# Performance work log

Hardware: AMD Instinct MI355X
Metric: run time of the kernel (lower is better)

The kernel has to match this reference:

```python
import jax, jax.numpy as jnp
import numpy as np

C = 256; G = 16; GC = C // G; K = 3; P = K * K
N = 4; H = 64; W = 64
PAD = 1; OFFSET_SCALE = 1.0; LN_EPS = 1e-5


def setup_inputs() -> dict:
    key = jax.random.key(0)
    ks = jax.random.split(key, 8)
    s = 0.02
    return {
        "x": jax.random.normal(ks[0], (N, C, H, W), jnp.float32),
        "dw_w": jax.random.normal(ks[1], (C, 1, K, K), jnp.float32) * s,
        "dw_b": jnp.zeros((C,), jnp.float32),
        "ln_g": jnp.ones((C,), jnp.float32),
        "ln_b": jnp.zeros((C,), jnp.float32),
        "off_w": jax.random.normal(ks[2], (C, G * P * 2), jnp.float32) * s,
        "off_b": jnp.zeros((G * P * 2,), jnp.float32),
        "mask_w": jax.random.normal(ks[3], (C, G * P), jnp.float32) * s,
        "mask_b": jnp.zeros((G * P,), jnp.float32),
        "inp_w": jax.random.normal(ks[4], (C, C), jnp.float32) * s,
        "inp_b": jnp.zeros((C,), jnp.float32),
        "out_w": jax.random.normal(ks[5], (C, C), jnp.float32) * s,
        "out_b": jnp.zeros((C,), jnp.float32),
    }


def _dcnv3_nchw(x, dw_w, dw_b, ln_g, ln_b, off_w, off_b, mask_w, mask_b,
                inp_w, inp_b, out_w, out_b):
    # NCHW -> NHWC (wrapper permute)
    xn = jnp.transpose(x, (0, 2, 3, 1))                      # (N,H,W,C)
    x_proj = xn @ inp_w + inp_b                              # input_proj

    # offset/mask branch: depthwise conv (NCHW) -> LayerNorm (channels-last) -> GELU
    x1 = jax.lax.conv_general_dilated(
        x, dw_w, window_strides=(1, 1), padding=((PAD, PAD), (PAD, PAD)),
        dimension_numbers=("NCHW", "OIHW", "NCHW"), feature_group_count=C)
    x1 = jnp.transpose(x1, (0, 2, 3, 1)) + dw_b
    mu = x1.mean(-1, keepdims=True)
    var = ((x1 - mu) ** 2).mean(-1, keepdims=True)
    x1 = (x1 - mu) * jax.lax.rsqrt(var + LN_EPS) * ln_g + ln_b
    x1 = jax.nn.gelu(x1, approximate=False)

    offset = (x1 @ off_w + off_b).reshape(N, H, W, G, P, 2)  # (x,y) pairs
    mask = jax.nn.softmax((x1 @ mask_w + mask_b).reshape(N, H, W, G, P), axis=-1)

    # pad sampled feature map with zeros (F.pad before sampling)
    xp = jnp.pad(x_proj, ((0, 0), (PAD, PAD), (PAD, PAD), (0, 0)))
    Hin, Win = H + 2 * PAD, W + 2 * PAD
    xg = xp.reshape(N, Hin, Win, G, GC)

    # reference points, normalized by padded size
    ref_y = (jnp.arange(H, dtype=jnp.float32) + PAD + 0.5) / Hin
    ref_x = (jnp.arange(W, dtype=jnp.float32) + PAD + 0.5) / Win
    ref = jnp.stack([jnp.broadcast_to(ref_x[None, :], (H, W)),
                     jnp.broadcast_to(ref_y[:, None], (H, W))], -1)  # (H,W,2)

    # dilation grid: x varies in the outer loop (torch meshgrid 'ij')
    d = jnp.arange(K, dtype=jnp.float32) - (K - 1) // 2     # [-1,0,1]
    gx = jnp.repeat(d, K) / Win
    gy = jnp.tile(d, K) / Hin
    grid = jnp.stack([gx, gy], -1)                           # (P,2)

    norm = jnp.array([Win, Hin], jnp.float32)
    loc = (ref[None, :, :, None, None, :] + grid * OFFSET_SCALE
           + offset * OFFSET_SCALE / norm)                   # (N,H,W,G,P,2)

    # grid_sample bilinear, align_corners=False, zero padding
    px = loc[..., 0] * Win - 0.5
    py = loc[..., 1] * Hin - 0.5
    x0 = jnp.floor(px); y0 = jnp.floor(py)
    wx = px - x0; wy = py - y0
    x0i = x0.astype(jnp.int32); y0i = y0.astype(jnp.int32)

    n_idx = jnp.arange(N)[:, None, None, None, None]
    g_idx = jnp.arange(G)[None, None, None, :, None]

    def corner(iy, ix, w):
        valid = (iy >= 0) & (iy < Hin) & (ix >= 0) & (ix < Win)
        v = xg[n_idx, jnp.clip(iy, 0, Hin - 1), jnp.clip(ix, 0, Win - 1), g_idx]
        wgt = jnp.where(valid, w, 0.0) * mask                # fold mask into weights
        return jnp.einsum("nhwgp,nhwgpc->nhwgc", wgt, v)

    out = (corner(y0i, x0i, (1 - wy) * (1 - wx))
           + corner(y0i, x0i + 1, (1 - wy) * wx)
           + corner(y0i + 1, x0i, wy * (1 - wx))
           + corner(y0i + 1, x0i + 1, wy * wx))               # (N,H,W,G,GC)

    out = out.reshape(N, H, W, C) @ out_w + out_b            # output_proj
    return jnp.transpose(out, (0, 3, 1, 2))                  # NHWC -> NCHW


def reference(x, dw_w, dw_b, ln_g, ln_b, off_w, off_b, mask_w, mask_b,
              inp_w, inp_b, out_w, out_b):
    return _dcnv3_nchw(x, dw_w, dw_b, ln_g, ln_b, off_w, off_b,
                       mask_w, mask_b, inp_w, inp_b, out_w, out_b)
```

## Files before the change

kernel.cpp:

```cpp
#include <hip/hip_runtime.h>
#include <hip/hip_bf16.h>
#include <math.h>


using bf16x8 = __attribute__((ext_vector_type(8))) short;
using f32x4  = __attribute__((ext_vector_type(4))) float;

#define GLOBAL_AS __attribute__((address_space(1)))
#define LDS_AS    __attribute__((address_space(3)))

static __device__ inline void g2lds16(const void* g, void* l) {
  __builtin_amdgcn_global_load_lds((const GLOBAL_AS int*)g, (LDS_AS int*)l, 16, 0, 0);
}
static __device__ inline unsigned short f2bf(float v) {
  __hip_bfloat16 b = __float2bfloat16(v);
  return *reinterpret_cast<unsigned short*>(&b);
}
static __device__ inline float us2f(unsigned short u) {
  union { unsigned u; float f; } c; c.u = ((unsigned)u) << 16; return c.f;
}

__global__ __launch_bounds__(256) void prep_w_k(
    const float* __restrict__ inp_w, const float* __restrict__ off_w,
    const float* __restrict__ off_b, const float* __restrict__ mask_w,
    const float* __restrict__ mask_b, const float* __restrict__ out_w,
    __hip_bfloat16* __restrict__ BtI, __hip_bfloat16* __restrict__ BtOM,
    __hip_bfloat16* __restrict__ BtO, float* __restrict__ bOM)
{
  const int b = blockIdx.x, t = threadIdx.x;
  if (b < 256) {
    int n = b;
    BtI[n * 256 + t] = __float2bfloat16(inp_w[t * 256 + n]);
  } else if (b < 768) {
    int n = b - 256;
    float v = 0.f;
    if (n < 288) v = off_w[t * 288 + n];
    else if (n < 432) v = mask_w[t * 144 + (n - 288)];
    BtOM[n * 256 + t] = __float2bfloat16(v);
    if (b == 256) {
      for (int idx = t; idx < 512; idx += 256) {
        float bv = (idx < 288) ? off_b[idx] : ((idx < 432) ? mask_b[idx - 288] : 0.f);
        bOM[idx] = bv;
      }
    }
  } else {
    int n = b - 768;
    BtO[n * 256 + t] = __float2bfloat16(out_w[t * 256 + n]);
  }
}

__global__ __launch_bounds__(1024) void stage2_gi_k(
    const float* __restrict__ x,
    const float* __restrict__ dw_w, const float* __restrict__ dw_b,
    const float* __restrict__ ln_g, const float* __restrict__ ln_b,
    const __hip_bfloat16* __restrict__ BtOM, const float* __restrict__ bOM,
    __hip_bfloat16* __restrict__ om,
    const __hip_bfloat16* __restrict__ BtI, const float* __restrict__ inp_b,
    __hip_bfloat16* __restrict__ xpu)
{
  __shared__ __align__(16) char smem[62464];
  const int bid = blockIdx.x;
  const int t = threadIdx.x;

  if (bid >= 256) {
    unsigned short* A = (unsigned short*)smem;
    float* ftile = (float*)(smem + 33792);
    short* Bs = (short*)(smem + 42112);

    const int strip = bid - 256;
    const int n4 = strip >> 6, hw0 = (strip & 63) * 64;
    const float* xb = x + (size_t)n4 * 1048576 + hw0;

    for (int ck = 0; ck < 8; ++ck) {
      const int ch0 = ck * 32;
      #pragma unroll
      for (int r = 0; r < 2; ++r) {
        int idx = t + r * 1024;
        int cl = idx >> 6, wl = idx & 63;
        ftile[cl * 65 + wl] = xb[(size_t)(ch0 + cl) * 4096 + wl];
      }
      __syncthreads();
      {
        int px = t >> 4, cq2 = t & 15;
        unsigned short b0 = f2bf(ftile[(cq2 * 2) * 65 + px]);
        unsigned short b1 = f2bf(ftile[(cq2 * 2 + 1) * 65 + px]);
        *(unsigned*)&A[px * 264 + ch0 + cq2 * 2] =
            (unsigned)b0 | ((unsigned)b1 << 16);
      }
      __syncthreads();
    }

    const int wave = t >> 6, lane = t & 63;
    const int quad = lane >> 4, lr = lane & 15;
    const int wm = wave >> 2, wn = wave & 3;
    f32x4 acc[4];
    #pragma unroll
    for (int i = 0; i < 4; ++i) acc[i] = (f32x4){0.f, 0.f, 0.f, 0.f};

    for (int kt = 0; kt < 256; kt += 32) {
      __syncthreads();
      {
        int col = t >> 2, kq = t & 3;
        g2lds16(BtI + (size_t)col * 256 + kt + kq * 8, (char*)Bs + t * 16);
      }
      __syncthreads();
      bf16x8 af = *(const bf16x8*)&A[(wm * 16 + lr) * 264 + kt + quad * 8];
      #pragma unroll
      for (int ni = 0; ni < 4; ++ni) {
        bf16x8 bf = *(const bf16x8*)&Bs[(wn * 64 + ni * 16 + lr) * 32 + quad * 8];
        acc[ni] = __builtin_amdgcn_mfma_f32_16x16x32_bf16(af, bf, acc[ni], 0, 0, 0);
      }
    }

    const size_t m0 = (size_t)strip * 64;
    #pragma unroll
    for (int ni = 0; ni < 4; ++ni) {
      int col = wn * 64 + ni * 16 + lr;
      float bv = inp_b[col];
      #pragma unroll
      for (int reg = 0; reg < 4; ++reg) {
        size_t m = m0 + wm * 16 + quad * 4 + reg;
        xpu[m * 256 + col] = __float2bfloat16(acc[ni][reg] + bv);
      }
    }
    return;
  }

  unsigned short* x1t = (unsigned short*)smem;
  float* psq  = (float*)(smem + 33792);
  float* murs = (float*)(smem + 41984);
  short* Bs   = (short*)(smem + 33792);

  const int blk = ((bid & 7) << 5) | (bid >> 3);
  const int n4 = blk >> 6, h = blk & 63;
  const int w = t & 63, q = t >> 6;

  const float* xb = x + (size_t)n4 * 1048576;
  const bool hm = (h > 0), hp = (h < 63);
  float av[16];
  float s1 = 0.f, s2 = 0.f;

  #pragma unroll 2
  for (int j = 0; j < 8; ++j) {
    #pragma unroll
    for (int u = 0; u < 2; ++u) {
      const int c = q * 16 + 2 * j + u;
      const float* xc = xb + (size_t)c * 4096 + h * 64 + w;
      float v0 = hm ? xc[-64] : 0.f;
      float v1 = xc[0];
      float v2 = hp ? xc[64] : 0.f;
      const float* wp = dw_w + c * 9;
      float a = dw_b[c];
      #pragma unroll
      for (int dh = 0; dh < 3; ++dh) {
        float v = (dh == 0) ? v0 : (dh == 1) ? v1 : v2;
        float vm = __shfl(v, w - 1, 64);
        float vp = __shfl(v, w + 1, 64);
        if (w == 0)  vm = 0.f;
        if (w == 63) vp = 0.f;
        a = fmaf(vm, wp[dh * 3 + 0], a);
        a = fmaf(v,  wp[dh * 3 + 1], a);
        a = fmaf(vp, wp[dh * 3 + 2], a);
      }
      s1 += a;
      s2 = fmaf(a, a, s2);
      av[2 * j + u] = a;
    }
  }

  psq[q * 64 + w] = s1;
  psq[1024 + q * 64 + w] = s2;
  __syncthreads();
  if (t < 64) {
    float a = 0.f, b = 0.f;
    #pragma unroll
    for (int j = 0; j < 16; ++j) { a += psq[j * 64 + t]; b += psq[1024 + j * 64 + t]; }
    float mu = a * (1.f / 256.f);
    murs[t] = mu;
    murs[64 + t] = rsqrtf(b * (1.f / 256.f) - mu * mu + 1e-5f);
  }
  __syncthreads();
  {
    float mu = murs[w], rs = murs[64 + w];
    #pragma unroll
    for (int j = 0; j < 8; ++j) {
      int c = q * 16 + 2 * j;
      float y0 = fmaf((av[2 * j] - mu) * rs, ln_g[c], ln_b[c]);
      float y1 = fmaf((av[2 * j + 1] - mu) * rs, ln_g[c + 1], ln_b[c + 1]);
      float g0 = 0.5f * y0 * (1.f + erff(y0 * 0.70710678f));
      float g1 = 0.5f * y1 * (1.f + erff(y1 * 0.70710678f));
      *(unsigned*)&x1t[w * 264 + c] = (unsigned)f2bf(g0) | ((unsigned)f2bf(g1) << 16);
    }
  }
  __syncthreads();

  const int wave = t >> 6, lane = t & 63;
  const int quad = lane >> 4, lr = lane & 15;
  const int wm = wave >> 2, wn = wave & 3;
  f32x4 acc[7];
  #pragma unroll
  for (int i = 0; i < 7; ++i) acc[i] = (f32x4){0.f, 0.f, 0.f, 0.f};

  for (int kt = 0; kt < 256; kt += 32) {
    __syncthreads();
    {
      int col = t >> 2, kq = t & 3;
      g2lds16(BtOM + (size_t)col * 256 + kt + kq * 8, (char*)Bs + t * 16);
      int jj = t + 1024;
      if (jj < 1792) {
        col = jj >> 2; kq = jj & 3;
        g2lds16(BtOM + (size_t)col * 256 + kt + kq * 8, (char*)Bs + jj * 16);
      }
    }
    __syncthreads();
    bf16x8 af = *(const bf16x8*)&x1t[(wm * 16 + lr) * 264 + kt + quad * 8];
    #pragma unroll
    for (int ni = 0; ni < 7; ++ni) {
      bf16x8 bf = *(const bf16x8*)&Bs[(wn * 112 + ni * 16 + lr) * 32 + quad * 8];
      acc[ni] = __builtin_amdgcn_mfma_f32_16x16x32_bf16(af, bf, acc[ni], 0, 0, 0);
    }
  }

  const size_t pix0 = (size_t)n4 * 4096 + (size_t)h * 64;
  #pragma unroll
  for (int ni = 0; ni < 7; ++ni) {
    int col = wn * 112 + ni * 16 + lr;
    if (col < 432) {
      float bv = bOM[col];
      #pragma unroll
      for (int reg = 0; reg < 4; ++reg) {
        int m = wm * 16 + quad * 4 + reg;
        om[(pix0 + m) * 448 + col] = __float2bfloat16(acc[ni][reg] + bv);
      }
    }
  }
}

__global__ __launch_bounds__(512) void fused_so_k(
    const __hip_bfloat16* __restrict__ xpu, const __hip_bfloat16* __restrict__ om,
    const __hip_bfloat16* __restrict__ BtO, const float* __restrict__ out_b,
    float* __restrict__ out)
{
  __shared__ __align__(16) char smem[33792];
  unsigned short* st = (unsigned short*)smem;
  short* Bs = (short*)(smem + 16896);

  const int bid = blockIdx.x;
  const int swz = ((bid & 7) << 6) | (bid >> 3);
  const int pix0 = swz << 5;
  const int t = threadIdx.x;

  {
    const int pl = t >> 4, g = t & 15;
    const int pix = pix0 + pl;
    const int n4s = pix >> 12;
    const int hw = pix & 4095;
    const int h = hw >> 6, w = hw & 63;
    const unsigned short* omp = (const unsigned short*)om + (size_t)pix * 448;

    float mk[9];
    {
      float mx = -1e30f;
      #pragma unroll
      for (int p = 0; p < 9; ++p) { mk[p] = us2f(omp[288 + g * 9 + p]); mx = fmaxf(mx, mk[p]); }
      float se = 0.f;
      #pragma unroll
      for (int p = 0; p < 9; ++p) { mk[p] = __expf(mk[p] - mx); se += mk[p]; }
      float inv = 1.f / se;
      #pragma unroll
      for (int p = 0; p < 9; ++p) mk[p] *= inv;
    }

    const __hip_bfloat16* xpg = xpu + (g << 4);
    float ax[16];
    #pragma unroll
    for (int i = 0; i < 16; ++i) ax[i] = 0.f;

    auto corner = [&](int iy, int ix, float wt) {
      if ((unsigned)(iy - 1) >= 64u || (unsigned)(ix - 1) >= 64u) return;
      const __hip_bfloat16* src =
          xpg + ((size_t)((n4s << 12) + (iy - 1) * 64 + (ix - 1)) << 8);
      uint4 u0 = *(const uint4*)src;
      uint4 u1 = *(const uint4*)(src + 8);
      const unsigned uu[8] = {u0.x, u0.y, u0.z, u0.w, u1.x, u1.y, u1.z, u1.w};
      #pragma unroll
      for (int i = 0; i < 8; ++i) {
        float lo = us2f((unsigned short)(uu[i] & 0xffff));
        float hi = us2f((unsigned short)(uu[i] >> 16));
        ax[2 * i + 0] = fmaf(wt, lo, ax[2 * i + 0]);
        ax[2 * i + 1] = fmaf(wt, hi, ax[2 * i + 1]);
      }
    };

    #pragma unroll
    for (int p = 0; p < 9; ++p) {
      float ox = us2f(omp[g * 18 + 2 * p]), oy = us2f(omp[g * 18 + 2 * p + 1]);
      float px = (float)(w + p / 3) + ox;
      float py = (float)(h + p % 3) + oy;
      float xf = floorf(px), yf = floorf(py);
      float wx = px - xf, wy = py - yf;
      int ix = (int)xf, iy = (int)yf;
      float m = mk[p];
      corner(iy,     ix,     (1.f - wy) * (1.f - wx) * m);
      corner(iy,     ix + 1, (1.f - wy) * wx * m);
      corner(iy + 1, ix,     wy * (1.f - wx) * m);
      corner(iy + 1, ix + 1, wy * wx * m);
    }

    unsigned short ub[16];
    #pragma unroll
    for (int i = 0; i < 16; ++i) ub[i] = f2bf(ax[i]);
    uint4 u0, u1;
    u0.x = (unsigned)ub[0] | ((unsigned)ub[1] << 16);
    u0.y = (unsigned)ub[2] | ((unsigned)ub[3] << 16);
    u0.z = (unsigned)ub[4] | ((unsigned)ub[5] << 16);
    u0.w = (unsigned)ub[6] | ((unsigned)ub[7] << 16);
    u1.x = (unsigned)ub[8] | ((unsigned)ub[9] << 16);
    u1.y = (unsigned)ub[10] | ((unsigned)ub[11] << 16);
    u1.z = (unsigned)ub[12] | ((unsigned)ub[13] << 16);
    u1.w = (unsigned)ub[14] | ((unsigned)ub[15] << 16);
    *(uint4*)&st[pl * 264 + g * 16] = u0;
    *(uint4*)&st[pl * 264 + g * 16 + 8] = u1;
  }

  const int wave = t >> 6, lane = t & 63;
  const int quad = lane >> 4, lr = lane & 15;
  const int wm = wave >> 2, wn = wave & 3;
  f32x4 acc[4];
  #pragma unroll
  for (int i = 0; i < 4; ++i) acc[i] = (f32x4){0.f, 0.f, 0.f, 0.f};

  for (int kt = 0; kt < 256; kt += 32) {
    __syncthreads();
    {
      #pragma unroll
      for (int r = 0; r < 2; ++r) {
        int j = t + r * 512;
        int col = j >> 2, kq = j & 3;
        g2lds16(BtO + (size_t)col * 256 + kt + kq * 8, (char*)Bs + j * 16);
      }
    }
    __syncthreads();
    bf16x8 af = *(const bf16x8*)&st[(wm * 16 + lr) * 264 + kt + quad * 8];
    #pragma unroll
    for (int ni = 0; ni < 4; ++ni) {
      bf16x8 bf = *(const bf16x8*)&Bs[(wn * 64 + ni * 16 + lr) * 32 + quad * 8];
      acc[ni] = __builtin_amdgcn_mfma_f32_16x16x32_bf16(af, bf, acc[ni], 0, 0, 0);
    }
  }

  const int n4 = pix0 >> 12, hw0 = pix0 & 4095;
  #pragma unroll
  for (int ni = 0; ni < 4; ++ni) {
    int col = wn * 64 + ni * 16 + lr;
    float bv = out_b[col];
    float4 v;
    v.x = acc[ni][0] + bv; v.y = acc[ni][1] + bv;
    v.z = acc[ni][2] + bv; v.w = acc[ni][3] + bv;
    *(float4*)&out[(size_t)(n4 * 256 + col) * 4096 + hw0 + wm * 16 + quad * 4] = v;
  }
}

extern "C" void kernel_launch(void* const* d_in, const int* in_sizes, int n_in,
                              void* d_out, int out_size, void* d_ws, size_t ws_size,
                              hipStream_t stream) {
  const float* x      = (const float*)d_in[0];
  const float* dw_w   = (const float*)d_in[1];
  const float* dw_b   = (const float*)d_in[2];
  const float* ln_g   = (const float*)d_in[3];
  const float* ln_b   = (const float*)d_in[4];
  const float* off_w  = (const float*)d_in[5];
  const float* off_b  = (const float*)d_in[6];
  const float* mask_w = (const float*)d_in[7];
  const float* mask_b = (const float*)d_in[8];
  const float* inp_w  = (const float*)d_in[9];
  const float* inp_b  = (const float*)d_in[10];
  const float* out_w  = (const float*)d_in[11];
  const float* out_b  = (const float*)d_in[12];
  float* out = (float*)d_out;

  char* w0 = (char*)d_ws;
  __hip_bfloat16* xpu  = (__hip_bfloat16*)(w0);
  __hip_bfloat16* om   = (__hip_bfloat16*)(w0 + 8388608);
  __hip_bfloat16* BtI  = (__hip_bfloat16*)(w0 + 23068672);
  __hip_bfloat16* BtOM = (__hip_bfloat16*)(w0 + 23199744);
  __hip_bfloat16* BtO  = (__hip_bfloat16*)(w0 + 23461888);
  float*          bOM  = (float*)(w0 + 23592960);
  if (ws_size < 23595008) return;

  prep_w_k<<<1024, 256, 0, stream>>>(inp_w, off_w, off_b, mask_w, mask_b,
                                     out_w, BtI, BtOM, BtO, bOM);
  stage2_gi_k<<<512, 1024, 0, stream>>>(x, dw_w, dw_b, ln_g, ln_b, BtOM, bOM,
                                        om, BtI, inp_b, xpu);
  fused_so_k<<<512, 512, 0, stream>>>(xpu, om, BtO, out_b, out);
}
```

Measured before the change: 156.8 us.

## Double-buffer weight tiles and preload A fragments in all three GEMM loops

Each of the three MFMA GEMM loops now stages the next 32-wide K slice of the weight matrix into an alternate LDS buffer with global_load_lds while the current slice is computed. This cuts the two barriers per step to one. The A operand fragments are loaded into registers once before the loop. The input-projection transpose also prefetches the next channel chunk of x into registers ahead of use. The costs are more LDS in the output kernel, more VGPRs for the held A fragments, and a possible race, since async LDS loads are only separated from readers by a single barrier.

Measured after the change: 152.2 us. 1.03x faster.

```diff
diff --git a/kernel.cpp b/kernel.cpp
--- a/kernel.cpp
+++ b/kernel.cpp
@@ -58,26 +58,30 @@
     const __hip_bfloat16* __restrict__ BtI, const float* __restrict__ inp_b,
     __hip_bfloat16* __restrict__ xpu)
 {
-  __shared__ __align__(16) char smem[62464];
+  __shared__ __align__(16) char smem[57344];
   const int bid = blockIdx.x;
   const int t = threadIdx.x;
 
   if (bid >= 256) {
     unsigned short* A = (unsigned short*)smem;
     float* ftile = (float*)(smem + 33792);
-    short* Bs = (short*)(smem + 42112);
 
     const int strip = bid - 256;
     const int n4 = strip >> 6, hw0 = (strip & 63) * 64;
     const float* xb = x + (size_t)n4 * 1048576 + hw0;
 
+    const int cl0 = t >> 6, wl0 = t & 63;
+    const int cl1 = (t + 1024) >> 6, wl1 = (t + 1024) & 63;
+    float p0 = xb[(size_t)cl0 * 4096 + wl0];
+    float p1 = xb[(size_t)cl1 * 4096 + wl1];
+
     for (int ck = 0; ck < 8; ++ck) {
       const int ch0 = ck * 32;
-      #pragma unroll
-      for (int r = 0; r < 2; ++r) {
-        int idx = t + r * 1024;
-        int cl = idx >> 6, wl = idx & 63;
-        ftile[cl * 65 + wl] = xb[(size_t)(ch0 + cl) * 4096 + wl];
+      ftile[cl0 * 65 + wl0] = p0;
+      ftile[cl1 * 65 + wl1] = p1;
+      if (ck < 7) {
+        p0 = xb[(size_t)(ch0 + 32 + cl0) * 4096 + wl0];
+        p1 = xb[(size_t)(ch0 + 32 + cl1) * 4096 + wl1];
       }
       __syncthreads();
       {
@@ -93,23 +97,37 @@
     const int wave = t >> 6, lane = t & 63;
     const int quad = lane >> 4, lr = lane & 15;
     const int wm = wave >> 2, wn = wave & 3;
+
+    bf16x8 areg[8];
+    #pragma unroll
+    for (int s = 0; s < 8; ++s)
+      areg[s] = *(const bf16x8*)&A[(wm * 16 + lr) * 264 + s * 32 + quad * 8];
+    __syncthreads();
+
+    auto stageI = [&](int s, int buf) {
+      int col = t >> 2, kq = t & 3;
+      g2lds16(BtI + (size_t)col * 256 + s * 32 + kq * 8,
+              smem + buf * 16384 + t * 16);
+    };
+
     f32x4 acc[4];
     #pragma unroll
     for (int i = 0; i < 4; ++i) acc[i] = (f32x4){0.f, 0.f, 0.f, 0.f};
 
-    for (int kt = 0; kt < 256; kt += 32) {
+    stageI(0, 0);
+    __syncthreads();
+    #pragma unroll
+    for (int s = 0; s < 8; ++s) {
+      if (s < 7) stageI(s + 1, (s + 1) & 1);
+      const short* B = (const short*)(smem + (s & 1) * 16384);
+      bf16x8 bfr[4];
+      #pragma unroll
+      for (int ni = 0; ni < 4; ++ni)
+        bfr[ni] = *(const bf16x8*)&B[(wn * 64 + ni * 16 + lr) * 32 + quad * 8];
+      #pragma unroll
+      for (int ni = 0; ni < 4; ++ni)
+        acc[ni] = __builtin_amdgcn_mfma_f32_16x16x32_bf16(areg[s], bfr[ni], acc[ni], 0, 0, 0);
       __syncthreads();
-      {
-        int col = t >> 2, kq = t & 3;
-        g2lds16(BtI + (size_t)col * 256 + kt + kq * 8, (char*)Bs + t * 16);
-      }
-      __syncthreads();
-      bf16x8 af = *(const bf16x8*)&A[(wm * 16 + lr) * 264 + kt + quad * 8];
-      #pragma unroll
-      for (int ni = 0; ni < 4; ++ni) {
-        bf16x8 bf = *(const bf16x8*)&Bs[(wn * 64 + ni * 16 + lr) * 32 + quad * 8];
-        acc[ni] = __builtin_amdgcn_mfma_f32_16x16x32_bf16(af, bf, acc[ni], 0, 0, 0);
-      }
     }
 
     const size_t m0 = (size_t)strip * 64;
@@ -129,7 +147,6 @@
   unsigned short* x1t = (unsigned short*)smem;
   float* psq  = (float*)(smem + 33792);
   float* murs = (float*)(smem + 41984);
-  short* Bs   = (short*)(smem + 33792);
 
   const int blk = ((bid & 7) << 5) | (bid >> 3);
   const int n4 = blk >> 6, h = blk & 63;
@@ -197,28 +214,42 @@
   const int wave = t >> 6, lane = t & 63;
   const int quad = lane >> 4, lr = lane & 15;
   const int wm = wave >> 2, wn = wave & 3;
+
+  bf16x8 areg[8];
+  #pragma unroll
+  for (int s = 0; s < 8; ++s)
+    areg[s] = *(const bf16x8*)&x1t[(wm * 16 + lr) * 264 + s * 32 + quad * 8];
+  __syncthreads();
+
+  auto stageOM = [&](int s, int buf) {
+    char* dst = smem + buf * 28672;
+    int col = t >> 2, kq = t & 3;
+    g2lds16(BtOM + (size_t)col * 256 + s * 32 + kq * 8, dst + t * 16);
+    int jj = t + 1024;
+    if (jj < 1792) {
+      int col2 = jj >> 2, kq2 = jj & 3;
+      g2lds16(BtOM + (size_t)col2 * 256 + s * 32 + kq2 * 8, dst + jj * 16);
+    }
+  };
+
   f32x4 acc[7];
   #pragma unroll
   for (int i = 0; i < 7; ++i) acc[i] = (f32x4){0.f, 0.f, 0.f, 0.f};
 
-  for (int kt = 0; kt < 256; kt += 32) {
+  stageOM(0, 0);
+  __syncthreads();
+  #pragma unroll
+  for (int s = 0; s < 8; ++s) {
+    if (s < 7) stageOM(s + 1, (s + 1) & 1);
+    const short* B = (const short*)(smem + (s & 1) * 28672);
+    bf16x8 bfr[7];
+    #pragma unroll
+    for (int ni = 0; ni < 7; ++ni)
+      bfr[ni] = *(const bf16x8*)&B[(wn * 112 + ni * 16 + lr) * 32 + quad * 8];
+    #pragma unroll
+    for (int ni = 0; ni < 7; ++ni)
+      acc[ni] = __builtin_amdgcn_mfma_f32_16x16x32_bf16(areg[s], bfr[ni], acc[ni], 0, 0, 0);
     __syncthreads();
-    {
-      int col = t >> 2, kq = t & 3;
-      g2lds16(BtOM + (size_t)col * 256 + kt + kq * 8, (char*)Bs + t * 16);
-      int jj = t + 1024;
-      if (jj < 1792) {
-        col = jj >> 2; kq = jj & 3;
-        g2lds16(BtOM + (size_t)col * 256 + kt + kq * 8, (char*)Bs + jj * 16);
-      }
-    }
-    __syncthreads();
-    bf16x8 af = *(const bf16x8*)&x1t[(wm * 16 + lr) * 264 + kt + quad * 8];
-    #pragma unroll
-    for (int ni = 0; ni < 7; ++ni) {
-      bf16x8 bf = *(const bf16x8*)&Bs[(wn * 112 + ni * 16 + lr) * 32 + quad * 8];
-      acc[ni] = __builtin_amdgcn_mfma_f32_16x16x32_bf16(af, bf, acc[ni], 0, 0, 0);
-    }
   }
 
   const size_t pix0 = (size_t)n4 * 4096 + (size_t)h * 64;
@@ -241,14 +272,25 @@
     const __hip_bfloat16* __restrict__ BtO, const float* __restrict__ out_b,
     float* __restrict__ out)
 {
-  __shared__ __align__(16) char smem[33792];
+  __shared__ __align__(16) char smem[49664];
   unsigned short* st = (unsigned short*)smem;
-  short* Bs = (short*)(smem + 16896);
 
   const int bid = blockIdx.x;
   const int swz = ((bid & 7) << 6) | (bid >> 3);
   const int pix0 = swz << 5;
   const int t = threadIdx.x;
+
+  auto stageO = [&](int s, int buf) {
+    char* dst = smem + 16896 + buf * 16384;
+    #pragma unroll
+    for (int r = 0; r < 2; ++r) {
+      int j = t + r * 512;
+      int col = j >> 2, kq = j & 3;
+      g2lds16(BtO + (size_t)col * 256 + s * 32 + kq * 8, dst + j * 16);
+    }
+  };
+
+  stageO(0, 0);
 
   {
     const int pl = t >> 4, g = t & 15;
@@ -322,31 +364,33 @@
     *(uint4*)&st[pl * 264 + g * 16] = u0;
     *(uint4*)&st[pl * 264 + g * 16 + 8] = u1;
   }
+  __syncthreads();
 
   const int wave = t >> 6, lane = t & 63;
   const int quad = lane >> 4, lr = lane & 15;
   const int wm = wave >> 2, wn = wave & 3;
+
+  bf16x8 areg[8];
+  #pragma unroll
+  for (int s = 0; s < 8; ++s)
+    areg[s] = *(const bf16x8*)&st[(wm * 16 + lr) * 264 + s * 32 + quad * 8];
+
   f32x4 acc[4];
   #pragma unroll
   for (int i = 0; i < 4; ++i) acc[i] = (f32x4){0.f, 0.f, 0.f, 0.f};
 
-  for (int kt = 0; kt < 256; kt += 32) {
+  #pragma unroll
+  for (int s = 0; s < 8; ++s) {
+    if (s < 7) stageO(s + 1, (s + 1) & 1);
+    const short* B = (const short*)(smem + 16896 + (s & 1) * 16384);
+    bf16x8 bfr[4];
+    #pragma unroll
+    for (int ni = 0; ni < 4; ++ni)
+      bfr[ni] = *(const bf16x8*)&B[(wn * 64 + ni * 16 + lr) * 32 + quad * 8];
+    #pragma unroll
+    for (int ni = 0; ni < 4; ++ni)
+      acc[ni] = __builtin_amdgcn_mfma_f32_16x16x32_bf16(areg[s], bfr[ni], acc[ni], 0, 0, 0);
     __syncthreads();
-    {
-      #pragma unroll
-      for (int r = 0; r < 2; ++r) {
-        int j = t + r * 512;
-        int col = j >> 2, kq = j & 3;
-        g2lds16(BtO + (size_t)col * 256 + kt + kq * 8, (char*)Bs + j * 16);
-      }
-    }
-    __syncthreads();
-    bf16x8 af = *(const bf16x8*)&st[(wm * 16 + lr) * 264 + kt + quad * 8];
-    #pragma unroll
-    for (int ni = 0; ni < 4; ++ni) {
-      bf16x8 bf = *(const bf16x8*)&Bs[(wn * 64 + ni * 16 + lr) * 32 + quad * 8];
-      acc[ni] = __builtin_amdgcn_mfma_f32_16x16x32_bf16(af, bf, acc[ni], 0, 0, 0);
-    }
   }
 
   const int n4 = pix0 >> 12, hw0 = pix0 & 4095;
```
